# Optimization experiments

Hardware: AMD Instinct MI355X
Metric: run time of the kernel (lower is better)

The kernel has to match this reference:

```python
import jax, jax.numpy as jnp
import numpy as np

D_MODEL = 1024
N_HEADS = 16
D_HEAD = D_MODEL // N_HEADS


def setup_inputs() -> dict:
    key = jax.random.key(0)
    ks = jax.random.split(key, 11)
    B, L = 2, 2048
    s = 1.0 / np.sqrt(D_MODEL)
    return {
        "query": jax.random.normal(ks[0], (B, L, D_MODEL), jnp.float32),
        "key": jax.random.normal(ks[1], (B, L, D_MODEL), jnp.float32),
        "value": jax.random.normal(ks[2], (B, L, D_MODEL), jnp.float32),
        "Wq": jax.random.normal(ks[3], (D_MODEL, D_MODEL), jnp.float32) * s,
        "bq": jnp.zeros((D_MODEL,), jnp.float32),
        "Wk": jax.random.normal(ks[4], (D_MODEL, D_MODEL), jnp.float32) * s,
        "bk": jnp.zeros((D_MODEL,), jnp.float32),
        "Wv": jax.random.normal(ks[5], (D_MODEL, D_MODEL), jnp.float32) * s,
        "bv": jnp.zeros((D_MODEL,), jnp.float32),
        "Wo": jax.random.normal(ks[6], (D_MODEL, D_MODEL), jnp.float32) * s,
        "bo": jnp.zeros((D_MODEL,), jnp.float32),
    }


def reference(query, key, value, Wq, bq, Wk, bk, Wv, bv, Wo, bo):
    B, Lq, _ = query.shape
    Lk = key.shape[1]
    scale = D_HEAD ** -0.5
    # projections; weights stored as [in, out] (torch Linear applies x @ W.T; here W is already transposed)
    q = (query @ Wq + bq).reshape(B, Lq, N_HEADS, D_HEAD).transpose(0, 2, 1, 3)  # [B,H,Lq,dh]
    k = (key @ Wk + bk).reshape(B, Lk, N_HEADS, D_HEAD).transpose(0, 2, 1, 3)
    v = (value @ Wv + bv).reshape(B, Lk, N_HEADS, D_HEAD).transpose(0, 2, 1, 3)
    scores = jnp.einsum('bhqd,bhkd->bhqk', q, k) * scale  # [B,H,Lq,Lk]
    # causal mask (is_causal=True)
    causal = jnp.triu(jnp.ones((Lq, Lk), dtype=bool), k=1)
    scores = jnp.where(causal, -jnp.inf, scores)
    attn = jax.nn.softmax(scores, axis=-1)
    out = jnp.einsum('bhqk,bhkd->bhqd', attn, v)  # [B,H,Lq,dh]
    out = out.transpose(0, 2, 1, 3).reshape(B, Lq, D_MODEL)
    return out @ Wo + bo
```

## Files before the change

kernel.cpp:

```cpp
#include <hip/hip_runtime.h>
#include <hip/hip_bf16.h>

typedef __bf16 bf16x8 __attribute__((ext_vector_type(8)));
typedef __bf16 bf16x4 __attribute__((ext_vector_type(4)));
typedef float floatx4 __attribute__((ext_vector_type(4)));

#define MFMA16(a, b, c) __builtin_amdgcn_mfma_f32_16x16x32_bf16(a, b, c, 0, 0, 0)
#define AS1 __attribute__((address_space(1)))
#define AS3 __attribute__((address_space(3)))

constexpr int D = 1024;
constexpr int L = 2048;
constexpr int BB = 2;
constexpr int DH = 64;
constexpr float NEG_BIG = -1e30f;
constexpr float SCALE_LOG2E = 0.125f * 1.4426950408889634f;

__device__ __forceinline__ void gld16(const __bf16* g, __bf16* l) {
  __builtin_amdgcn_global_load_lds((AS1 void*)g, (AS3 void*)l, 16, 0, 0);
}

__global__ __launch_bounds__(256) void cvt_x(const float* __restrict__ xq, const float* __restrict__ xk,
                                             const float* __restrict__ xv, __bf16* __restrict__ out) {
  const int z = blockIdx.z;
  const float* src = z == 0 ? xq : z == 1 ? xk : xv;
  __bf16* dst = out + (size_t)z * BB * L * D;
  const int N = BB * L * D;
  const int stride = gridDim.x * 256 * 4;
  for (int i = (blockIdx.x * 256 + threadIdx.x) * 4; i < N; i += stride) {
    float4 f = *(const float4*)&src[i];
    bf16x4 b = {(__bf16)f.x, (__bf16)f.y, (__bf16)f.z, (__bf16)f.w};
    *(bf16x4*)&dst[i] = b;
  }
}

__global__ void transpose_w(const float* __restrict__ w0, const float* __restrict__ w1,
                            const float* __restrict__ w2, const float* __restrict__ w3,
                            __bf16* __restrict__ out) {
  __shared__ __bf16 tile[32][33];
  int mat = blockIdx.z;
  const float* src = mat == 0 ? w0 : mat == 1 ? w1 : mat == 2 ? w2 : w3;
  __bf16* dst = out + (size_t)mat * D * D;
  int bx = blockIdx.x * 32, by = blockIdx.y * 32;
  int tx = threadIdx.x, ty = threadIdx.y;
#pragma unroll
  for (int i = 0; i < 32; i += 8)
    tile[ty + i][tx] = (__bf16)src[(size_t)(by + ty + i) * D + bx + tx];
  __syncthreads();
#pragma unroll
  for (int i = 0; i < 32; i += 8)
    dst[(size_t)(bx + ty + i) * D + by + tx] = tile[tx][ty + i];
}

__device__ __forceinline__ void stage_tile(const __bf16* __restrict__ A, const __bf16* __restrict__ Bt,
                                           __bf16* sA, __bf16* sB, int m0, int n0, int kb,
                                           int lr, int lc) {
  gld16(&A[(size_t)(m0 + lr) * 1024 + kb + lc],       &sA[lr * 32 + lc]);
  gld16(&A[(size_t)(m0 + 64 + lr) * 1024 + kb + lc],  &sA[(64 + lr) * 32 + lc]);
  gld16(&Bt[(size_t)(n0 + lr) * 1024 + kb + lc],      &sB[lr * 32 + lc]);
  gld16(&Bt[(size_t)(n0 + 64 + lr) * 1024 + kb + lc], &sB[(64 + lr) * 32 + lc]);
}

__device__ __forceinline__ void gemm_core(const __bf16* __restrict__ A, const __bf16* __restrict__ Bt,
                                          __bf16 (&sA)[2][128 * 32], __bf16 (&sB)[2][128 * 32],
                                          int m0, int n0, int wm, int wn, int l15, int quad, int t,
                                          floatx4 (&acc)[4][4]) {
  const int lr = t >> 2;
  const int lc = (t & 3) * 8;

  stage_tile(A, Bt, sA[0], sB[0], m0, n0, 0, lr, lc);
  __syncthreads();

  int cur = 0;
  for (int kb = 0; kb < 1024; kb += 32) {
    if (kb < 1024 - 32)
      stage_tile(A, Bt, sA[cur ^ 1], sB[cur ^ 1], m0, n0, kb + 32, lr, lc);

    bf16x8 af[4], bf_[4];
#pragma unroll
    for (int i = 0; i < 4; i++)
      af[i] = *(const bf16x8*)&sA[cur][(wm * 64 + i * 16 + l15) * 32 + quad * 8];
#pragma unroll
    for (int j = 0; j < 4; j++)
      bf_[j] = *(const bf16x8*)&sB[cur][(wn * 64 + j * 16 + l15) * 32 + quad * 8];
#pragma unroll
    for (int i = 0; i < 4; i++)
#pragma unroll
      for (int j = 0; j < 4; j++)
        acc[i][j] = MFMA16(af[i], bf_[j], acc[i][j]);

    __syncthreads();
    cur ^= 1;
  }
}

__global__ __launch_bounds__(256) void gemm_proj(const __bf16* __restrict__ xc, const __bf16* __restrict__ wt,
                                                 const float* __restrict__ bq, const float* __restrict__ bk,
                                                 const float* __restrict__ bv, __bf16* __restrict__ qkv) {
  __shared__ __align__(16) __bf16 sA[2][128 * 32];
  __shared__ __align__(16) __bf16 sB[2][128 * 32];

  const int flat = (blockIdx.z * 32 + blockIdx.y) * 8 + blockIdx.x;
  const int s = (flat & 7) * 96 + (flat >> 3);
  const int z = s >> 8;
  const int rem = s & 255;
  const int by = rem >> 3, bx = rem & 7;

  const __bf16* A = xc + (size_t)z * BB * L * D;
  const __bf16* Bt = wt + (size_t)z * D * D;
  const float* bias = z == 0 ? bq : z == 1 ? bk : bv;
  __bf16* dst = qkv + (size_t)z * BB * L * D;

  const int t = threadIdx.x;
  const int lane = t & 63;
  const int w = t >> 6;
  const int wm = w >> 1, wn = w & 1;
  const int l15 = lane & 15, quad = lane >> 4;
  const int m0 = by * 128, n0 = bx * 128;

  floatx4 acc[4][4];
#pragma unroll
  for (int i = 0; i < 4; i++)
#pragma unroll
    for (int j = 0; j < 4; j++) acc[i][j] = (floatx4){0.f, 0.f, 0.f, 0.f};

  gemm_core(A, Bt, sA, sB, m0, n0, wm, wn, l15, quad, t, acc);

  float bvv[4];
#pragma unroll
  for (int j = 0; j < 4; j++) bvv[j] = bias[n0 + wn * 64 + j * 16 + l15];

#pragma unroll
  for (int i = 0; i < 4; i++) {
    const int rowb = m0 + wm * 64 + i * 16 + quad * 4;
#pragma unroll
    for (int j = 0; j < 4; j++) {
      const int col = n0 + wn * 64 + j * 16 + l15;
      const int h = col >> 6, d = col & 63;
#pragma unroll
      for (int rr = 0; rr < 4; rr++) {
        float val = acc[i][j][rr] + bvv[j];
        const int row = rowb + rr;
        const int b = row >> 11, l = row & 2047;
        if (z == 0) {
          val *= SCALE_LOG2E;
          dst[((size_t)(b * 16 + h) * 2048 + l) * 64 + d] = (__bf16)val;
        } else if (z == 1) {
          dst[((size_t)(b * 16 + h) * 2048 + l) * 64 + d] = (__bf16)val;
        } else {
          dst[((size_t)(b * 16 + h) * 64 + d) * 2048 + l] = (__bf16)val;
        }
      }
    }
  }
}

__global__ __launch_bounds__(256) void gemm_o(const __bf16* __restrict__ ctx, const __bf16* __restrict__ wto,
                                              const float* __restrict__ bo, float* __restrict__ out) {
  __shared__ __align__(16) __bf16 sA[2][128 * 32];
  __shared__ __align__(16) __bf16 sB[2][128 * 32];

  const int flat = blockIdx.y * 8 + blockIdx.x;
  const int s = (flat & 7) * 32 + (flat >> 3);
  const int by = s >> 3, bx = s & 7;

  const int t = threadIdx.x;
  const int lane = t & 63;
  const int w = t >> 6;
  const int wm = w >> 1, wn = w & 1;
  const int l15 = lane & 15, quad = lane >> 4;
  const int m0 = by * 128, n0 = bx * 128;

  floatx4 acc[4][4];
#pragma unroll
  for (int i = 0; i < 4; i++)
#pragma unroll
    for (int j = 0; j < 4; j++) acc[i][j] = (floatx4){0.f, 0.f, 0.f, 0.f};

  gemm_core(ctx, wto, sA, sB, m0, n0, wm, wn, l15, quad, t, acc);

  float bvv[4];
#pragma unroll
  for (int j = 0; j < 4; j++) bvv[j] = bo[n0 + wn * 64 + j * 16 + l15];

#pragma unroll
  for (int i = 0; i < 4; i++) {
    const int rowb = m0 + wm * 64 + i * 16 + quad * 4;
#pragma unroll
    for (int j = 0; j < 4; j++) {
      const int col = n0 + wn * 64 + j * 16 + l15;
#pragma unroll
      for (int rr = 0; rr < 4; rr++)
        out[(size_t)(rowb + rr) * 1024 + col] = acc[i][j][rr] + bvv[j];
    }
  }
}

__global__ __launch_bounds__(256, 4) void flash_attn(const __bf16* __restrict__ q, const __bf16* __restrict__ k,
                                                     const __bf16* __restrict__ vT, __bf16* __restrict__ ctx) {
  __shared__ __align__(16) __bf16 kbuf[2][4096];
  __shared__ __align__(16) __bf16 vbuf[2][4096];

  const int t = threadIdx.x;
  const int lane = t & 63;
  const int w = t >> 6;
  const int l15 = lane & 15, quad = lane >> 4;
  const int bh = blockIdx.y;
  const int qt = (blockIdx.x + blockIdx.y) & 31;
  const int q0 = qt * 64;

  const __bf16* qb = q + (size_t)bh * L * DH;
  const __bf16* kb_ = k + (size_t)bh * L * DH;
  const __bf16* vb = vT + (size_t)bh * DH * L;

  const int qg = q0 + w * 16;
  const int qrow = qg + l15;
  bf16x8 aq0 = *(const bf16x8*)&qb[(size_t)qrow * 64 + quad * 8];
  bf16x8 aq1 = *(const bf16x8*)&qb[(size_t)qrow * 64 + 32 + quad * 8];

  const int c0 = t, c1 = 256 + t;
  const int kr0 = c0 >> 3, kd0 = ((c0 & 7) ^ (kr0 & 7)) * 8;
  const int kr1 = c1 >> 3, kd1 = ((c1 & 7) ^ (kr1 & 7)) * 8;

  floatx4 o[4];
#pragma unroll
  for (int nt = 0; nt < 4; nt++) o[nt] = (floatx4){0.f, 0.f, 0.f, 0.f};
  float psum = 0.f;

  {
    gld16(&kb_[(size_t)kr0 * 64 + kd0], &kbuf[0][c0 * 8]);
    gld16(&kb_[(size_t)kr1 * 64 + kd1], &kbuf[0][c1 * 8]);
    gld16(&vb[(size_t)kr0 * L + kd0],   &vbuf[0][c0 * 8]);
    gld16(&vb[(size_t)kr1 * L + kd1],   &vbuf[0][c1 * 8]);
  }
  __syncthreads();

  for (int it = 0; it <= qt; ++it) {
    const int cur = it & 1;
    const int kt = it * 64;

    if (it < qt) {
      const int ktn = kt + 64;
      gld16(&kb_[(size_t)(ktn + kr0) * 64 + kd0], &kbuf[cur ^ 1][c0 * 8]);
      gld16(&kb_[(size_t)(ktn + kr1) * 64 + kd1], &kbuf[cur ^ 1][c1 * 8]);
      gld16(&vb[(size_t)kr0 * L + ktn + kd0],     &vbuf[cur ^ 1][c0 * 8]);
      gld16(&vb[(size_t)kr1 * L + ktn + kd1],     &vbuf[cur ^ 1][c1 * 8]);
    }

    const bool diag = (it == qt);

#pragma unroll
    for (int sp = 0; sp < 2; ++sp) {
      floatx4 z[2];
#pragma unroll
      for (int u = 0; u < 2; ++u) {
        const int kr = (2 * sp + u) * 16 + l15;
        bf16x8 kf0 = *(const bf16x8*)&kbuf[cur][(kr * 8 + (quad ^ (kr & 7))) * 8];
        bf16x8 kf1 = *(const bf16x8*)&kbuf[cur][(kr * 8 + ((quad + 4) ^ (kr & 7))) * 8];
        floatx4 zz = (floatx4){0.f, 0.f, 0.f, 0.f};
        zz = MFMA16(kf0, aq0, zz);
        zz = MFMA16(kf1, aq1, zz);
        z[u] = zz;
      }

      if (diag) {
#pragma unroll
        for (int u = 0; u < 2; ++u) {
          const int kgb = kt + (2 * sp + u) * 16 + quad * 4;
#pragma unroll
          for (int rr = 0; rr < 4; rr++)
            if (kgb + rr > qrow) z[u][rr] = NEG_BIG;
        }
      }

      bf16x8 pa;
#pragma unroll
      for (int u = 0; u < 2; ++u)
#pragma unroll
        for (int rr = 0; rr < 4; rr++) {
          const float p = __builtin_amdgcn_exp2f(z[u][rr]);
          psum += p;
          pa[u * 4 + rr] = (__bf16)p;
        }

#pragma unroll
      for (int nt = 0; nt < 4; nt++) {
        const int d = nt * 16 + l15;
        const int x0 = (sp * 4 + (quad >> 1)) ^ (d & 7);
        const int x1 = (sp * 4 + 2 + (quad >> 1)) ^ (d & 7);
        union { bf16x8 v8; bf16x4 v4[2]; } uv;
        uv.v4[0] = *(const bf16x4*)&vbuf[cur][(d * 8 + x0) * 8 + (quad & 1) * 4];
        uv.v4[1] = *(const bf16x4*)&vbuf[cur][(d * 8 + x1) * 8 + (quad & 1) * 4];
        o[nt] = MFMA16(pa, uv.v8, o[nt]);
      }
    }
    __syncthreads();
  }

  psum += __shfl_xor(psum, 16);
  psum += __shfl_xor(psum, 32);
  const float invs = 1.f / psum;

  const int b = bh >> 4, h = bh & 15;
#pragma unroll
  for (int rr = 0; rr < 4; rr++) {
    const float inv = __shfl(invs, (lane & 48) + quad * 4 + rr);
    const int row = qg + quad * 4 + rr;
#pragma unroll
    for (int nt = 0; nt < 4; nt++) {
      const int col = h * 64 + nt * 16 + l15;
      ctx[((size_t)b * L + row) * 1024 + col] = (__bf16)(o[nt][rr] * inv);
    }
  }
}

extern "C" void kernel_launch(void* const* d_in, const int* in_sizes, int n_in,
                              void* d_out, int out_size, void* d_ws, size_t ws_size,
                              hipStream_t stream) {
  const float* x_q = (const float*)d_in[0];
  const float* x_k = (const float*)d_in[1];
  const float* x_v = (const float*)d_in[2];
  const float* Wq  = (const float*)d_in[3];
  const float* bq  = (const float*)d_in[4];
  const float* Wk  = (const float*)d_in[5];
  const float* bk  = (const float*)d_in[6];
  const float* Wv  = (const float*)d_in[7];
  const float* bv  = (const float*)d_in[8];
  const float* Wo  = (const float*)d_in[9];
  const float* bo  = (const float*)d_in[10];

  char* ws = (char*)d_ws;
  __bf16* xc  = (__bf16*)ws;
  __bf16* wt  = (__bf16*)(ws + ((size_t)24 << 20));
  __bf16* qkv = (__bf16*)(ws + ((size_t)32 << 20));
  __bf16* ctx = (__bf16*)ws;
  __bf16* qp  = qkv;
  __bf16* kp  = qkv + (size_t)BB * L * D;
  __bf16* vtp = qkv + (size_t)2 * BB * L * D;

  cvt_x<<<dim3(1024, 1, 3), 256, 0, stream>>>(x_q, x_k, x_v, xc);
  transpose_w<<<dim3(32, 32, 4), dim3(32, 8), 0, stream>>>(Wq, Wk, Wv, Wo, wt);
  gemm_proj<<<dim3(8, 32, 3), 256, 0, stream>>>(xc, wt, bq, bk, bv, qkv);
  flash_attn<<<dim3(32, 32), 256, 0, stream>>>(qp, kp, vtp, ctx);
  gemm_o<<<dim3(8, 32), 256, 0, stream>>>(ctx, wt + (size_t)3 * D * D, bo, (float*)d_out);
}
```

Baseline: 233.0 us.

## Use single-buffered K=64 GEMM tiles with XOR-swizzled LDS and occupancy hint

The projection and output GEMMs drop the double-buffered K=32 staging in favour of a single buffer with K=64 per step. An XOR swizzle on the source column avoids LDS bank conflicts on the fragment reads. The step count halves and each step issues two MFMA groups, and launch_bounds(256,3) asks for three blocks per CU so other waves can hide load latency. The trade-off is that loads no longer overlap compute inside a block, since each iteration waits on its own stage before computing.

Measured after the change: 225.7 us. 1.03x faster.

```diff
diff --git a/kernel.cpp b/kernel.cpp
--- a/kernel.cpp
+++ b/kernel.cpp
@@ -52,53 +52,61 @@
     dst[(size_t)(bx + ty + i) * D + by + tx] = tile[tx][ty + i];
 }
 
-__device__ __forceinline__ void stage_tile(const __bf16* __restrict__ A, const __bf16* __restrict__ Bt,
-                                           __bf16* sA, __bf16* sB, int m0, int n0, int kb,
-                                           int lr, int lc) {
-  gld16(&A[(size_t)(m0 + lr) * 1024 + kb + lc],       &sA[lr * 32 + lc]);
-  gld16(&A[(size_t)(m0 + 64 + lr) * 1024 + kb + lc],  &sA[(64 + lr) * 32 + lc]);
-  gld16(&Bt[(size_t)(n0 + lr) * 1024 + kb + lc],      &sB[lr * 32 + lc]);
-  gld16(&Bt[(size_t)(n0 + 64 + lr) * 1024 + kb + lc], &sB[(64 + lr) * 32 + lc]);
+__device__ __forceinline__ void stage64(const __bf16* __restrict__ A, const __bf16* __restrict__ Bt,
+                                        __bf16* sA, __bf16* sB, int m0, int n0, int kb,
+                                        int rl, int dstc, int srcc) {
+#pragma unroll
+  for (int g = 0; g < 4; g++) {
+    const int r = g * 32 + rl;
+    gld16(&A[(size_t)(m0 + r) * 1024 + kb + srcc],  &sA[r * 64 + dstc]);
+    gld16(&Bt[(size_t)(n0 + r) * 1024 + kb + srcc], &sB[r * 64 + dstc]);
+  }
 }
 
 __device__ __forceinline__ void gemm_core(const __bf16* __restrict__ A, const __bf16* __restrict__ Bt,
-                                          __bf16 (&sA)[2][128 * 32], __bf16 (&sB)[2][128 * 32],
+                                          __bf16* sA, __bf16* sB,
                                           int m0, int n0, int wm, int wn, int l15, int quad, int t,
                                           floatx4 (&acc)[4][4]) {
-  const int lr = t >> 2;
-  const int lc = (t & 3) * 8;
-
-  stage_tile(A, Bt, sA[0], sB[0], m0, n0, 0, lr, lc);
-  __syncthreads();
-
-  int cur = 0;
-  for (int kb = 0; kb < 1024; kb += 32) {
-    if (kb < 1024 - 32)
-      stage_tile(A, Bt, sA[cur ^ 1], sB[cur ^ 1], m0, n0, kb + 32, lr, lc);
-
-    bf16x8 af[4], bf_[4];
-#pragma unroll
-    for (int i = 0; i < 4; i++)
-      af[i] = *(const bf16x8*)&sA[cur][(wm * 64 + i * 16 + l15) * 32 + quad * 8];
-#pragma unroll
-    for (int j = 0; j < 4; j++)
-      bf_[j] = *(const bf16x8*)&sB[cur][(wn * 64 + j * 16 + l15) * 32 + quad * 8];
-#pragma unroll
-    for (int i = 0; i < 4; i++)
-#pragma unroll
-      for (int j = 0; j < 4; j++)
-        acc[i][j] = MFMA16(af[i], bf_[j], acc[i][j]);
-
+  const int rl = t >> 3;
+  const int dstc = (t & 7) * 8;
+  const int srcc = ((t & 7) ^ (rl & 7)) * 8;
+  const int x7 = l15 & 7;
+
+  for (int kb = 0; kb < 1024; kb += 64) {
+    stage64(A, Bt, sA, sB, m0, n0, kb, rl, dstc, srcc);
     __syncthreads();
-    cur ^= 1;
-  }
-}
-
-__global__ __launch_bounds__(256) void gemm_proj(const __bf16* __restrict__ xc, const __bf16* __restrict__ wt,
-                                                 const float* __restrict__ bq, const float* __restrict__ bk,
-                                                 const float* __restrict__ bv, __bf16* __restrict__ qkv) {
-  __shared__ __align__(16) __bf16 sA[2][128 * 32];
-  __shared__ __align__(16) __bf16 sB[2][128 * 32];
+
+    bf16x8 af[2][4], bf_[2][4];
+#pragma unroll
+    for (int kk = 0; kk < 2; kk++) {
+#pragma unroll
+      for (int i = 0; i < 4; i++) {
+        const int row = wm * 64 + i * 16 + l15;
+        af[kk][i] = *(const bf16x8*)&sA[(row * 8 + ((kk * 4 + quad) ^ x7)) * 8];
+      }
+#pragma unroll
+      for (int j = 0; j < 4; j++) {
+        const int row = wn * 64 + j * 16 + l15;
+        bf_[kk][j] = *(const bf16x8*)&sB[(row * 8 + ((kk * 4 + quad) ^ x7)) * 8];
+      }
+    }
+#pragma unroll
+    for (int kk = 0; kk < 2; kk++)
+#pragma unroll
+      for (int i = 0; i < 4; i++)
+#pragma unroll
+        for (int j = 0; j < 4; j++)
+          acc[i][j] = MFMA16(af[kk][i], bf_[kk][j], acc[i][j]);
+
+    __syncthreads();
+  }
+}
+
+__global__ __launch_bounds__(256, 3) void gemm_proj(const __bf16* __restrict__ xc, const __bf16* __restrict__ wt,
+                                                    const float* __restrict__ bq, const float* __restrict__ bk,
+                                                    const float* __restrict__ bv, __bf16* __restrict__ qkv) {
+  __shared__ __align__(16) __bf16 sA[128 * 64];
+  __shared__ __align__(16) __bf16 sB[128 * 64];
 
   const int flat = (blockIdx.z * 32 + blockIdx.y) * 8 + blockIdx.x;
   const int s = (flat & 7) * 96 + (flat >> 3);
@@ -155,10 +163,10 @@
   }
 }
 
-__global__ __launch_bounds__(256) void gemm_o(const __bf16* __restrict__ ctx, const __bf16* __restrict__ wto,
-                                              const float* __restrict__ bo, float* __restrict__ out) {
-  __shared__ __align__(16) __bf16 sA[2][128 * 32];
-  __shared__ __align__(16) __bf16 sB[2][128 * 32];
+__global__ __launch_bounds__(256, 3) void gemm_o(const __bf16* __restrict__ ctx, const __bf16* __restrict__ wto,
+                                                 const float* __restrict__ bo, float* __restrict__ out) {
+  __shared__ __align__(16) __bf16 sA[128 * 64];
+  __shared__ __align__(16) __bf16 sB[128 * 64];
 
   const int flat = blockIdx.y * 8 + blockIdx.x;
   const int s = (flat & 7) * 32 + (flat >> 3);
```

## Swizzle GEMM LDS tiles and replace syncthreads with explicit waitcnt barriers

Applied to the files above, without the earlier changes.

Applies an XOR swizzle to the 16-byte chunks written into shared memory by the GEMM staging loads and to the fragment reads, aiming to remove LDS bank conflicts. The double-buffered loop now uses explicit vmcnt/lgkmcnt waits and raw s_barrier calls, so only the current tile's global-to-LDS loads are waited on and the next tile's prefetch stays in flight. It also adds a minimum-occupancy hint of 3 blocks per SM to both GEMM kernels. The hand-written waitcnt values depend on the exact number of outstanding loads, and the occupancy hint may force register spilling.

Measured after the change: 228.6 us. No clear change (-1.9%).

```diff
diff --git a/kernel.cpp b/kernel.cpp
--- a/kernel.cpp
+++ b/kernel.cpp
@@ -52,51 +52,64 @@
     dst[(size_t)(bx + ty + i) * D + by + tx] = tile[tx][ty + i];
 }
 
-__device__ __forceinline__ void stage_tile(const __bf16* __restrict__ A, const __bf16* __restrict__ Bt,
-                                           __bf16* sA, __bf16* sB, int m0, int n0, int kb,
-                                           int lr, int lc) {
-  gld16(&A[(size_t)(m0 + lr) * 1024 + kb + lc],       &sA[lr * 32 + lc]);
-  gld16(&A[(size_t)(m0 + 64 + lr) * 1024 + kb + lc],  &sA[(64 + lr) * 32 + lc]);
-  gld16(&Bt[(size_t)(n0 + lr) * 1024 + kb + lc],      &sB[lr * 32 + lc]);
-  gld16(&Bt[(size_t)(n0 + 64 + lr) * 1024 + kb + lc], &sB[(64 + lr) * 32 + lc]);
+__device__ __forceinline__ void stage32(const __bf16* __restrict__ A, const __bf16* __restrict__ Bt,
+                                        __bf16* sA, __bf16* sB, int m0, int n0, int kb,
+                                        int r, int sc, int dst) {
+  gld16(&A[(size_t)(m0 + r) * 1024 + kb + sc],       &sA[dst]);
+  gld16(&A[(size_t)(m0 + 64 + r) * 1024 + kb + sc],  &sA[2048 + dst]);
+  gld16(&Bt[(size_t)(n0 + r) * 1024 + kb + sc],      &sB[dst]);
+  gld16(&Bt[(size_t)(n0 + 64 + r) * 1024 + kb + sc], &sB[2048 + dst]);
 }
 
 __device__ __forceinline__ void gemm_core(const __bf16* __restrict__ A, const __bf16* __restrict__ Bt,
                                           __bf16 (&sA)[2][128 * 32], __bf16 (&sB)[2][128 * 32],
                                           int m0, int n0, int wm, int wn, int l15, int quad, int t,
                                           floatx4 (&acc)[4][4]) {
-  const int lr = t >> 2;
-  const int lc = (t & 3) * 8;
-
-  stage_tile(A, Bt, sA[0], sB[0], m0, n0, 0, lr, lc);
-  __syncthreads();
+  const int r = t >> 2;
+  const int sc = ((t & 3) ^ ((r >> 1) & 3)) * 8;
+  const int dst = t * 8;
+  const int sw2 = (l15 >> 1) & 3;
+
+  stage32(A, Bt, sA[0], sB[0], m0, n0, 0, r, sc, dst);
 
   int cur = 0;
   for (int kb = 0; kb < 1024; kb += 32) {
-    if (kb < 1024 - 32)
-      stage_tile(A, Bt, sA[cur ^ 1], sB[cur ^ 1], m0, n0, kb + 32, lr, lc);
+    if (kb + 32 < 1024) {
+      stage32(A, Bt, sA[cur ^ 1], sB[cur ^ 1], m0, n0, kb + 32, r, sc, dst);
+      asm volatile("s_waitcnt vmcnt(4)" ::: "memory");
+    } else {
+      asm volatile("s_waitcnt vmcnt(0)" ::: "memory");
+    }
+    __builtin_amdgcn_s_barrier();
 
     bf16x8 af[4], bf_[4];
 #pragma unroll
-    for (int i = 0; i < 4; i++)
-      af[i] = *(const bf16x8*)&sA[cur][(wm * 64 + i * 16 + l15) * 32 + quad * 8];
-#pragma unroll
-    for (int j = 0; j < 4; j++)
-      bf_[j] = *(const bf16x8*)&sB[cur][(wn * 64 + j * 16 + l15) * 32 + quad * 8];
+    for (int i = 0; i < 4; i++) {
+      const int row = wm * 64 + i * 16 + l15;
+      af[i] = *(const bf16x8*)&sA[cur][(row * 4 + (quad ^ sw2)) * 8];
+    }
+#pragma unroll
+    for (int j = 0; j < 4; j++) {
+      const int row = wn * 64 + j * 16 + l15;
+      bf_[j] = *(const bf16x8*)&sB[cur][(row * 4 + (quad ^ sw2)) * 8];
+    }
+    asm volatile("s_waitcnt lgkmcnt(0)" ::: "memory");
+    __builtin_amdgcn_sched_barrier(0);
+    __builtin_amdgcn_s_barrier();
+
 #pragma unroll
     for (int i = 0; i < 4; i++)
 #pragma unroll
       for (int j = 0; j < 4; j++)
         acc[i][j] = MFMA16(af[i], bf_[j], acc[i][j]);
 
-    __syncthreads();
     cur ^= 1;
   }
 }
 
-__global__ __launch_bounds__(256) void gemm_proj(const __bf16* __restrict__ xc, const __bf16* __restrict__ wt,
-                                                 const float* __restrict__ bq, const float* __restrict__ bk,
-                                                 const float* __restrict__ bv, __bf16* __restrict__ qkv) {
+__global__ __launch_bounds__(256, 3) void gemm_proj(const __bf16* __restrict__ xc, const __bf16* __restrict__ wt,
+                                                    const float* __restrict__ bq, const float* __restrict__ bk,
+                                                    const float* __restrict__ bv, __bf16* __restrict__ qkv) {
   __shared__ __align__(16) __bf16 sA[2][128 * 32];
   __shared__ __align__(16) __bf16 sB[2][128 * 32];
 
@@ -155,8 +168,8 @@
   }
 }
 
-__global__ __launch_bounds__(256) void gemm_o(const __bf16* __restrict__ ctx, const __bf16* __restrict__ wto,
-                                              const float* __restrict__ bo, float* __restrict__ out) {
+__global__ __launch_bounds__(256, 3) void gemm_o(const __bf16* __restrict__ ctx, const __bf16* __restrict__ wto,
+                                                 const float* __restrict__ bo, float* __restrict__ out) {
   __shared__ __align__(16) __bf16 sA[2][128 * 32];
   __shared__ __align__(16) __bf16 sB[2][128 * 32];
 
```
